# Optimization experiments

Hardware: AMD Instinct MI355X
Metric: run time of the kernel (lower is better)

The kernel has to match this reference:

```python
import jax, jax.numpy as jnp
import numpy as np
from jax import lax

SPARSITY_WEIGHT = 0.7
BETA_A = 1.0
BETA_I = 1.0
B, N, ZI, ZA = 32, 1024, 64, 128
EPS = 1e-10


def setup_inputs() -> dict:
    key = jax.random.key(0)
    ks = jax.random.split(key, 11)
    A_hat_batch = jax.random.uniform(ks[0], (B, N, N), jnp.float32, 1e-6, 1.0 - 1e-6)
    A_true = jax.random.bernoulli(ks[1], 0.05, (B, N, N)).astype(jnp.float32)
    X_hat = jnp.zeros((1,), jnp.float32)
    X_true = jnp.zeros((1,), jnp.float32)
    mu_A = jax.random.normal(ks[2], (B, ZA), jnp.float32)
    logvar_A = 0.5 * jax.random.normal(ks[3], (B, ZA), jnp.float32)
    mu_i = jax.random.normal(ks[4], (B, N, ZI), jnp.float32)
    logvar_i = 0.5 * jax.random.normal(ks[5], (B, N, ZI), jnp.float32)
    z_a = jax.random.normal(ks[6], (B, ZA), jnp.float32)
    all_B_mus = jax.random.normal(ks[7], (N, ZI, ZA), jnp.float32) * 0.1
    all_B_logvars = jax.random.normal(ks[8], (N, ZI, ZA), jnp.float32) * 0.1
    return dict(A_hat_batch=A_hat_batch, A_true=A_true, X_hat=X_hat, X_true=X_true,
                mu_A=mu_A, logvar_A=logvar_A, mu_i=mu_i, logvar_i=logvar_i,
                z_a=z_a, all_B_mus=all_B_mus, all_B_logvars=all_B_logvars)


def kl_between_two_gaussians(m1, lv1, m2, lv2):
    # Faithful to original (note: 0.5 multiplies only det ratio, and -d not -0.5*log-det form)
    det_term = jnp.exp(lv1.sum(-1) - lv2.sum(-1))  # det1/det2
    d_term = m1.shape[-1]
    trace_term = jnp.exp(lv1 - lv2).sum(-1)
    inner_prod_term = (jnp.square(m2 - m1) / jnp.exp(lv2)).sum(-1)
    return 0.5 * det_term - d_term + trace_term + inner_prod_term


def adj_recon_term(A_hat, A_true):
    A = jnp.where(A_hat == 0.0, EPS, jnp.where(A_hat == 1.0, 1.0 - EPS, A_hat))
    ll = A_true * jnp.log(A) + (1.0 - A_true) * jnp.log(1.0 - A)
    ll = jnp.where(A_true == 0.0, ll * SPARSITY_WEIGHT, ll)
    return ll.sum((-1, -2)).mean()


def reference(A_hat_batch, A_true, X_hat, X_true, mu_A, logvar_A, mu_i, logvar_i, z_a, all_B_mus, all_B_logvars):
    A_recon = adj_recon_term(A_hat_batch, A_true)
    X_recon = 0.0
    # KL_A: to standard normal prior
    zeros = jnp.zeros_like(mu_A)
    KL_A = kl_between_two_gaussians(mu_A, logvar_A, zeros, zeros).mean()
    # KL_i: vectorized over node axis (original looped per node)
    z_a_d = lax.stop_gradient(z_a)
    prior_means = lax.stop_gradient(jnp.einsum('nfg,bg->bnf', all_B_mus, z_a_d))
    prior_logvars = lax.stop_gradient(jnp.einsum('nfg,bg->bnf', all_B_logvars, z_a_d))
    node_kls = kl_between_two_gaussians(mu_i, logvar_i, prior_means, prior_logvars)  # [B, N]
    KL_i = node_kls.sum(-1).mean()
    neg_beta_elbo = -(A_recon + X_recon + BETA_A * KL_A + BETA_I * KL_i)
    return (A_recon, KL_A, KL_i, neg_beta_elbo)
```

## Files before the change

kernel.cpp:

```cpp
#include <hip/hip_runtime.h>


static constexpr int BB = 32;
static constexpr int NN = 1024;
static constexpr int ZIc = 64;
static constexpr int ZAc = 128;
static constexpr int NV4 = (BB * NN * NN) / 4;
static constexpr int ABLOCKS = 2048;

#define EPSV 1e-10f
#define SPW 0.7f

__device__ __forceinline__ float ll_elem(float a, float t) {
    a = (a == 0.0f) ? EPSV : ((a == 1.0f) ? (1.0f - EPSV) : a);
    float la  = __logf(a);
    float l1a = __logf(1.0f - a);
    float v = t * la + (1.0f - t) * l1a;
    return (t == 0.0f) ? SPW * v : v;
}

__global__ __launch_bounds__(256) void arecon_kernel(
        const float4* __restrict__ Ah, const float4* __restrict__ At,
        double* __restrict__ slots) {
    float lsum = 0.0f;
    const int stride = gridDim.x * blockDim.x;
    for (int i = blockIdx.x * blockDim.x + threadIdx.x; i < NV4; i += stride) {
        float4 a = Ah[i];
        float4 t = At[i];
        lsum += ll_elem(a.x, t.x);
        lsum += ll_elem(a.y, t.y);
        lsum += ll_elem(a.z, t.z);
        lsum += ll_elem(a.w, t.w);
    }
#pragma unroll
    for (int m = 1; m < 64; m <<= 1) lsum += __shfl_xor(lsum, m, 64);
    __shared__ float wsum[4];
    const int lane = threadIdx.x & 63, wv = threadIdx.x >> 6;
    if (lane == 0) wsum[wv] = lsum;
    __syncthreads();
    if (threadIdx.x == 0)
        slots[blockIdx.x] = (double)(wsum[0] + wsum[1] + wsum[2] + wsum[3]);
}

__global__ __launch_bounds__(256) void kli_kernel(
        const float* __restrict__ mu_i, const float* __restrict__ lv_i,
        const float* __restrict__ z_a,
        const float* __restrict__ Bmu, const float* __restrict__ Blv,
        double* __restrict__ slots) {
    const int n    = blockIdx.x;
    const int wave = threadIdx.x >> 6;
    const int f    = threadIdx.x & 63;

    const float4* bmu = reinterpret_cast<const float4*>(Bmu + ((size_t)n * ZIc + f) * ZAc);
    const float4* blv = reinterpret_cast<const float4*>(Blv + ((size_t)n * ZIc + f) * ZAc);

    float pm[8], pl[8];
#pragma unroll
    for (int i = 0; i < 8; ++i) { pm[i] = 0.0f; pl[i] = 0.0f; }

    for (int c = 0; c < 8; ++c) {
        float4 m[4], l[4];
#pragma unroll
        for (int q = 0; q < 4; ++q) { m[q] = bmu[c * 4 + q]; l[q] = blv[c * 4 + q]; }
#pragma unroll
        for (int bi = 0; bi < 8; ++bi) {
            const int b = bi * 4 + wave;
            const float* z = z_a + b * ZAc + c * 16;
#pragma unroll
            for (int q = 0; q < 4; ++q) {
                float4 zz = *reinterpret_cast<const float4*>(z + q * 4);
                pm[bi] += m[q].x * zz.x + m[q].y * zz.y + m[q].z * zz.z + m[q].w * zz.w;
                pl[bi] += l[q].x * zz.x + l[q].y * zz.y + l[q].z * zz.z + l[q].w * zz.w;
            }
        }
    }

    double local = 0.0;
#pragma unroll
    for (int bi = 0; bi < 8; ++bi) {
        const int b = bi * 4 + wave;
        const size_t base = ((size_t)b * NN + n) * ZIc + f;
        float m1  = mu_i[base];
        float lv1 = lv_i[base];
        float d   = lv1 - pl[bi];
        float tr  = __expf(d);
        float dm  = pm[bi] - m1;
        float inn = dm * dm * __expf(-pl[bi]);
        float sd = d, st = tr, si = inn;
#pragma unroll
        for (int m = 1; m < 64; m <<= 1) {
            sd += __shfl_xor(sd, m, 64);
            st += __shfl_xor(st, m, 64);
            si += __shfl_xor(si, m, 64);
        }
        if (f == 0)
            local += (double)(0.5f * __expf(sd) - 64.0f + st + si);
    }
    __shared__ double wacc[4];
    if (f == 0) wacc[wave] = local;
    __syncthreads();
    if (threadIdx.x == 0)
        slots[n] = wacc[0] + wacc[1] + wacc[2] + wacc[3];
}

__global__ __launch_bounds__(64) void kla_kernel(
        const float* __restrict__ mu_A, const float* __restrict__ lv_A,
        double* __restrict__ slots) {
    const int b = blockIdx.x;
    const int lane = threadIdx.x;
    float lv0 = lv_A[b * ZAc + lane], lv1 = lv_A[b * ZAc + 64 + lane];
    float m0  = mu_A[b * ZAc + lane], m1  = mu_A[b * ZAc + 64 + lane];
    float slv = lv0 + lv1;
    float str = __expf(lv0) + __expf(lv1);
    float sin_ = m0 * m0 + m1 * m1;
#pragma unroll
    for (int m = 1; m < 64; m <<= 1) {
        slv  += __shfl_xor(slv, m, 64);
        str  += __shfl_xor(str, m, 64);
        sin_ += __shfl_xor(sin_, m, 64);
    }
    if (lane == 0)
        slots[b] = (double)(0.5f * __expf(slv) - 128.0f + str + sin_);
}

__global__ __launch_bounds__(256) void finalize_kernel(
        const double* __restrict__ ws, float* __restrict__ out) {
    double a = 0.0, ki = 0.0, ka = 0.0;
    for (int i = threadIdx.x; i < ABLOCKS; i += 256) a  += ws[i];
    for (int i = threadIdx.x; i < 1024;    i += 256) ki += ws[ABLOCKS + i];
    if (threadIdx.x < 32) ka = ws[ABLOCKS + 1024 + threadIdx.x];
#pragma unroll
    for (int m = 1; m < 64; m <<= 1) {
        a  += __shfl_xor(a, m, 64);
        ki += __shfl_xor(ki, m, 64);
        ka += __shfl_xor(ka, m, 64);
    }
    __shared__ double sa[4], ski[4], ska[4];
    const int lane = threadIdx.x & 63, wv = threadIdx.x >> 6;
    if (lane == 0) { sa[wv] = a; ski[wv] = ki; ska[wv] = ka; }
    __syncthreads();
    if (threadIdx.x == 0) {
        double A  = (sa[0] + sa[1] + sa[2] + sa[3]) / 32.0;
        double KI = (ski[0] + ski[1] + ski[2] + ski[3]) / 32.0;
        double KA = (ska[0] + ska[1] + ska[2] + ska[3]) / 32.0;
        out[0] = (float)A;
        out[1] = (float)KA;
        out[2] = (float)KI;
        out[3] = (float)(-(A + KA + KI));
    }
}

extern "C" void kernel_launch(void* const* d_in, const int* in_sizes, int n_in,
                              void* d_out, int out_size, void* d_ws, size_t ws_size,
                              hipStream_t stream) {
    const float* Ah   = (const float*)d_in[0];
    const float* At   = (const float*)d_in[1];
    const float* mu_A = (const float*)d_in[4];
    const float* lv_A = (const float*)d_in[5];
    const float* mu_i = (const float*)d_in[6];
    const float* lv_i = (const float*)d_in[7];
    const float* z_a  = (const float*)d_in[8];
    const float* Bmu  = (const float*)d_in[9];
    const float* Blv  = (const float*)d_in[10];

    double* ws = (double*)d_ws;
    float* out = (float*)d_out;

    hipLaunchKernelGGL(arecon_kernel, dim3(ABLOCKS), dim3(256), 0, stream,
                       (const float4*)Ah, (const float4*)At, ws);
    hipLaunchKernelGGL(kli_kernel, dim3(1024), dim3(256), 0, stream,
                       mu_i, lv_i, z_a, Bmu, Blv, ws + ABLOCKS);
    hipLaunchKernelGGL(kla_kernel, dim3(32), dim3(64), 0, stream,
                       mu_A, lv_A, ws + ABLOCKS + 1024);
    hipLaunchKernelGGL(finalize_kernel, dim3(1), dim3(256), 0, stream, ws, out);
}
```

Measured before the change: 407.1 us.

## Fuse recon and KL kernels into one launch with single-log likelihood

Merges the adjacency reconstruction and per-node KL kernels into one grid whose first blocks stream A_hat/A_true and whose remaining blocks compute the node KL terms. The KL_A computation moves into the finalize kernel, cutting the launch count from four to two. The log-likelihood now evaluates one log per element by selecting a or 1-a from the binary target. The KL path stages z_a in shared memory and merges two shuffle reductions into one. The aim is to reduce launch and tail overhead, let the two workloads overlap, and halve transcendental work. The single-log form is exact only when A_true is strictly 0 or 1.

```diff
diff --git a/kernel.cpp b/kernel.cpp
--- a/kernel.cpp
+++ b/kernel.cpp
@@ -1,143 +1,158 @@
 #include <hip/hip_runtime.h>
 
 
-static constexpr int BB = 32;
-static constexpr int NN = 1024;
+static constexpr int BB  = 32;
+static constexpr int NN  = 1024;
 static constexpr int ZIc = 64;
 static constexpr int ZAc = 128;
+static constexpr int AB  = 2048;
+static constexpr int KB  = 1024;
 static constexpr int NV4 = (BB * NN * NN) / 4;
-static constexpr int ABLOCKS = 2048;
 
 #define EPSV 1e-10f
-#define SPW 0.7f
+#define SPW  0.7f
 
 __device__ __forceinline__ float ll_elem(float a, float t) {
     a = (a == 0.0f) ? EPSV : ((a == 1.0f) ? (1.0f - EPSV) : a);
-    float la  = __logf(a);
-    float l1a = __logf(1.0f - a);
-    float v = t * la + (1.0f - t) * l1a;
-    return (t == 0.0f) ? SPW * v : v;
+    float x = (t == 0.0f) ? (1.0f - a) : a;
+    float s = (t == 0.0f) ? SPW : 1.0f;
+    return s * __logf(x);
 }
 
-__global__ __launch_bounds__(256) void arecon_kernel(
+__global__ __launch_bounds__(256, 4) void mega_kernel(
         const float4* __restrict__ Ah, const float4* __restrict__ At,
-        double* __restrict__ slots) {
-    float lsum = 0.0f;
-    const int stride = gridDim.x * blockDim.x;
-    for (int i = blockIdx.x * blockDim.x + threadIdx.x; i < NV4; i += stride) {
-        float4 a = Ah[i];
-        float4 t = At[i];
-        lsum += ll_elem(a.x, t.x);
-        lsum += ll_elem(a.y, t.y);
-        lsum += ll_elem(a.z, t.z);
-        lsum += ll_elem(a.w, t.w);
-    }
-#pragma unroll
-    for (int m = 1; m < 64; m <<= 1) lsum += __shfl_xor(lsum, m, 64);
-    __shared__ float wsum[4];
-    const int lane = threadIdx.x & 63, wv = threadIdx.x >> 6;
-    if (lane == 0) wsum[wv] = lsum;
-    __syncthreads();
-    if (threadIdx.x == 0)
-        slots[blockIdx.x] = (double)(wsum[0] + wsum[1] + wsum[2] + wsum[3]);
-}
-
-__global__ __launch_bounds__(256) void kli_kernel(
         const float* __restrict__ mu_i, const float* __restrict__ lv_i,
         const float* __restrict__ z_a,
         const float* __restrict__ Bmu, const float* __restrict__ Blv,
         double* __restrict__ slots) {
-    const int n    = blockIdx.x;
+    __shared__ float  zlds[BB * ZAc];
+    __shared__ double dred[4];
+    const int lane = threadIdx.x & 63;
     const int wave = threadIdx.x >> 6;
-    const int f    = threadIdx.x & 63;
 
-    const float4* bmu = reinterpret_cast<const float4*>(Bmu + ((size_t)n * ZIc + f) * ZAc);
-    const float4* blv = reinterpret_cast<const float4*>(Blv + ((size_t)n * ZIc + f) * ZAc);
+    if (blockIdx.x < AB) {
+        float lsum = 0.0f;
+        size_t tb = (size_t)blockIdx.x * 1024 + threadIdx.x;
+#pragma unroll 2
+        for (int s = 0; s < 4; ++s) {
+            float4 a[4], t[4];
+#pragma unroll
+            for (int k = 0; k < 4; ++k) a[k] = Ah[tb + 256 * k];
+#pragma unroll
+            for (int k = 0; k < 4; ++k) t[k] = At[tb + 256 * k];
+#pragma unroll
+            for (int k = 0; k < 4; ++k) {
+                lsum += ll_elem(a[k].x, t[k].x);
+                lsum += ll_elem(a[k].y, t[k].y);
+                lsum += ll_elem(a[k].z, t[k].z);
+                lsum += ll_elem(a[k].w, t[k].w);
+            }
+            tb += (size_t)AB * 1024;
+        }
+#pragma unroll
+        for (int m = 1; m < 64; m <<= 1) lsum += __shfl_xor(lsum, m, 64);
+        if (lane == 0) dred[wave] = (double)lsum;
+        __syncthreads();
+        if (threadIdx.x == 0)
+            slots[blockIdx.x] = dred[0] + dred[1] + dred[2] + dred[3];
+    } else {
+        const int n = blockIdx.x - AB;
+        const int f = lane;
+        {
+            const float4* z4 = reinterpret_cast<const float4*>(z_a);
+            float4* zl4 = reinterpret_cast<float4*>(zlds);
+#pragma unroll
+            for (int k = 0; k < 4; ++k)
+                zl4[k * 256 + threadIdx.x] = z4[k * 256 + threadIdx.x];
+        }
+        __syncthreads();
+        const float4* zl4 = reinterpret_cast<const float4*>(zlds);
 
-    float pm[8], pl[8];
+        const float4* bmu = reinterpret_cast<const float4*>(Bmu + ((size_t)n * ZIc + f) * ZAc);
+        const float4* blv = reinterpret_cast<const float4*>(Blv + ((size_t)n * ZIc + f) * ZAc);
+
+        float pm[8], pl[8];
 #pragma unroll
-    for (int i = 0; i < 8; ++i) { pm[i] = 0.0f; pl[i] = 0.0f; }
+        for (int i = 0; i < 8; ++i) { pm[i] = 0.0f; pl[i] = 0.0f; }
 
-    for (int c = 0; c < 8; ++c) {
-        float4 m[4], l[4];
+#pragma unroll 1
+        for (int c = 0; c < 8; ++c) {
+            float4 m[4], l[4];
 #pragma unroll
-        for (int q = 0; q < 4; ++q) { m[q] = bmu[c * 4 + q]; l[q] = blv[c * 4 + q]; }
+            for (int q = 0; q < 4; ++q) { m[q] = bmu[c * 4 + q]; l[q] = blv[c * 4 + q]; }
+#pragma unroll
+            for (int bi = 0; bi < 8; ++bi) {
+                const int b = bi * 4 + wave;
+#pragma unroll
+                for (int q = 0; q < 4; ++q) {
+                    float4 zz = zl4[b * 32 + c * 4 + q];
+                    pm[bi] += m[q].x * zz.x + m[q].y * zz.y + m[q].z * zz.z + m[q].w * zz.w;
+                    pl[bi] += l[q].x * zz.x + l[q].y * zz.y + l[q].z * zz.z + l[q].w * zz.w;
+                }
+            }
+        }
+
+        double local = 0.0;
 #pragma unroll
         for (int bi = 0; bi < 8; ++bi) {
             const int b = bi * 4 + wave;
-            const float* z = z_a + b * ZAc + c * 16;
+            const size_t base = ((size_t)b * NN + n) * ZIc + f;
+            float m1  = mu_i[base];
+            float lv1 = lv_i[base];
+            float d   = lv1 - pl[bi];
+            float dm  = pm[bi] - m1;
+            float sc  = __expf(d) + dm * dm * __expf(-pl[bi]);
+            float sd  = d;
 #pragma unroll
-            for (int q = 0; q < 4; ++q) {
-                float4 zz = *reinterpret_cast<const float4*>(z + q * 4);
-                pm[bi] += m[q].x * zz.x + m[q].y * zz.y + m[q].z * zz.z + m[q].w * zz.w;
-                pl[bi] += l[q].x * zz.x + l[q].y * zz.y + l[q].z * zz.z + l[q].w * zz.w;
+            for (int m = 1; m < 64; m <<= 1) {
+                sd += __shfl_xor(sd, m, 64);
+                sc += __shfl_xor(sc, m, 64);
             }
+            if (f == 0)
+                local += (double)(0.5f * __expf(sd) - 64.0f + sc);
         }
+        if (f == 0) dred[wave] = local;
+        __syncthreads();
+        if (threadIdx.x == 0)
+            slots[AB + n] = dred[0] + dred[1] + dred[2] + dred[3];
     }
-
-    double local = 0.0;
-#pragma unroll
-    for (int bi = 0; bi < 8; ++bi) {
-        const int b = bi * 4 + wave;
-        const size_t base = ((size_t)b * NN + n) * ZIc + f;
-        float m1  = mu_i[base];
-        float lv1 = lv_i[base];
-        float d   = lv1 - pl[bi];
-        float tr  = __expf(d);
-        float dm  = pm[bi] - m1;
-        float inn = dm * dm * __expf(-pl[bi]);
-        float sd = d, st = tr, si = inn;
-#pragma unroll
-        for (int m = 1; m < 64; m <<= 1) {
-            sd += __shfl_xor(sd, m, 64);
-            st += __shfl_xor(st, m, 64);
-            si += __shfl_xor(si, m, 64);
-        }
-        if (f == 0)
-            local += (double)(0.5f * __expf(sd) - 64.0f + st + si);
-    }
-    __shared__ double wacc[4];
-    if (f == 0) wacc[wave] = local;
-    __syncthreads();
-    if (threadIdx.x == 0)
-        slots[n] = wacc[0] + wacc[1] + wacc[2] + wacc[3];
-}
-
-__global__ __launch_bounds__(64) void kla_kernel(
-        const float* __restrict__ mu_A, const float* __restrict__ lv_A,
-        double* __restrict__ slots) {
-    const int b = blockIdx.x;
-    const int lane = threadIdx.x;
-    float lv0 = lv_A[b * ZAc + lane], lv1 = lv_A[b * ZAc + 64 + lane];
-    float m0  = mu_A[b * ZAc + lane], m1  = mu_A[b * ZAc + 64 + lane];
-    float slv = lv0 + lv1;
-    float str = __expf(lv0) + __expf(lv1);
-    float sin_ = m0 * m0 + m1 * m1;
-#pragma unroll
-    for (int m = 1; m < 64; m <<= 1) {
-        slv  += __shfl_xor(slv, m, 64);
-        str  += __shfl_xor(str, m, 64);
-        sin_ += __shfl_xor(sin_, m, 64);
-    }
-    if (lane == 0)
-        slots[b] = (double)(0.5f * __expf(slv) - 128.0f + str + sin_);
 }
 
 __global__ __launch_bounds__(256) void finalize_kernel(
-        const double* __restrict__ ws, float* __restrict__ out) {
-    double a = 0.0, ki = 0.0, ka = 0.0;
-    for (int i = threadIdx.x; i < ABLOCKS; i += 256) a  += ws[i];
-    for (int i = threadIdx.x; i < 1024;    i += 256) ki += ws[ABLOCKS + i];
-    if (threadIdx.x < 32) ka = ws[ABLOCKS + 1024 + threadIdx.x];
+        const double* __restrict__ ws,
+        const float* __restrict__ mu_A, const float* __restrict__ lv_A,
+        float* __restrict__ out) {
+    const int lane = threadIdx.x & 63;
+    const int wave = threadIdx.x >> 6;
+
+    double a = 0.0, ki = 0.0;
+    for (int i = threadIdx.x; i < AB; i += 256) a  += ws[i];
+    for (int i = threadIdx.x; i < KB; i += 256) ki += ws[AB + i];
 #pragma unroll
     for (int m = 1; m < 64; m <<= 1) {
         a  += __shfl_xor(a, m, 64);
         ki += __shfl_xor(ki, m, 64);
-        ka += __shfl_xor(ka, m, 64);
     }
+
+    double ka = 0.0;
+#pragma unroll 1
+    for (int bb = 0; bb < 8; ++bb) {
+        const int b = wave * 8 + bb;
+        float lv0 = lv_A[b * ZAc + lane], lv1 = lv_A[b * ZAc + 64 + lane];
+        float m0  = mu_A[b * ZAc + lane], m1  = mu_A[b * ZAc + 64 + lane];
+        float slv = lv0 + lv1;
+        float sc  = __expf(lv0) + __expf(lv1) + m0 * m0 + m1 * m1;
+#pragma unroll
+        for (int m = 1; m < 64; m <<= 1) {
+            slv += __shfl_xor(slv, m, 64);
+            sc  += __shfl_xor(sc, m, 64);
+        }
+        if (lane == 0)
+            ka += (double)(0.5f * __expf(slv) - 128.0f + sc);
+    }
+
     __shared__ double sa[4], ski[4], ska[4];
-    const int lane = threadIdx.x & 63, wv = threadIdx.x >> 6;
-    if (lane == 0) { sa[wv] = a; ski[wv] = ki; ska[wv] = ka; }
+    if (lane == 0) { sa[wave] = a; ski[wave] = ki; ska[wave] = ka; }
     __syncthreads();
     if (threadIdx.x == 0) {
         double A  = (sa[0] + sa[1] + sa[2] + sa[3]) / 32.0;
@@ -166,11 +181,9 @@
     double* ws = (double*)d_ws;
     float* out = (float*)d_out;
 
-    hipLaunchKernelGGL(arecon_kernel, dim3(ABLOCKS), dim3(256), 0, stream,
-                       (const float4*)Ah, (const float4*)At, ws);
-    hipLaunchKernelGGL(kli_kernel, dim3(1024), dim3(256), 0, stream,
-                       mu_i, lv_i, z_a, Bmu, Blv, ws + ABLOCKS);
-    hipLaunchKernelGGL(kla_kernel, dim3(32), dim3(64), 0, stream,
-                       mu_A, lv_A, ws + ABLOCKS + 1024);
-    hipLaunchKernelGGL(finalize_kernel, dim3(1), dim3(256), 0, stream, ws, out);
+    hipLaunchKernelGGL(mega_kernel, dim3(AB + KB), dim3(256), 0, stream,
+                       (const float4*)Ah, (const float4*)At,
+                       mu_i, lv_i, z_a, Bmu, Blv, ws);
+    hipLaunchKernelGGL(finalize_kernel, dim3(1), dim3(256), 0, stream,
+                       ws, mu_A, lv_A, out);
 }
```

New measurement: 452.2 us. 11.1% more time.
